# Performance work log

Hardware: AMD Instinct MI355X
Metric: run time of the kernel (lower is better)

## Reference

```python
import jax, jax.numpy as jnp
import numpy as np

B, L, F, H, HDE, E, V, MH, MW, TOUT = 64, 2, 512, 512, 512, 512, 94, 6, 40, 30
V2 = V + 2          # vocab + START/END + NULL slots
T = TOUT + 2        # decode steps
HW = MH * MW
START = V + 1
END = V + 1


def setup_inputs() -> dict:
    key = jax.random.key(0)
    ks = jax.random.split(key, 20)
    s = 0.05  # weight scale for numerical stability
    n = lambda k, shape: jax.random.normal(k, shape, jnp.float32) * s
    d = {}
    d['conv_f'] = jax.random.normal(ks[0], (B, F, MH, MW), jnp.float32)
    d['target'] = jax.random.randint(ks[1], (B, TOUT), 0, 95, dtype=jnp.int32)
    d['w_ih_en'] = n(ks[2], (L, 4 * H, F))
    d['w_hh_en'] = n(ks[3], (L, 4 * H, H))
    d['b_ih_en'] = n(ks[4], (L, 4 * H))
    d['b_hh_en'] = n(ks[5], (L, 4 * H))
    d['embed_w'] = n(ks[6], (V2, H))
    d['w_ih_de'] = n(ks[7], (L, 4 * HDE, H))
    d['w_hh_de'] = n(ks[8], (L, 4 * HDE, HDE))
    d['b_ih_de'] = n(ks[9], (L, 4 * HDE))
    d['b_hh_de'] = n(ks[10], (L, 4 * HDE))
    d['att_wh'] = n(ks[11], (E, HDE))
    d['att_bh'] = n(ks[12], (E,))
    d['att_conv_w'] = n(ks[13], (E, F, 3, 3))
    d['att_conv_b'] = n(ks[14], (E,))
    d['att_wv'] = n(ks[15], (1, E))
    d['att_bv'] = n(ks[16], (1,))
    d['out_w'] = n(ks[17], (V2, HDE + F))
    d['out_b'] = n(ks[18], (V2,))
    return d


def _lstm_cell(x, h, c, wih, whh, bih, bhh):
    # PyTorch gate order: i, f, g, o
    g = x @ wih.T + h @ whh.T + bih + bhh
    i, f, gg, o = jnp.split(g, 4, axis=-1)
    c_new = jax.nn.sigmoid(f) * c + jax.nn.sigmoid(i) * jnp.tanh(gg)
    h_new = jax.nn.sigmoid(o) * jnp.tanh(c_new)
    return h_new, c_new


def _forward(conv_f, target, w_ih_en, w_hh_en, b_ih_en, b_hh_en, embed_w,
             w_ih_de, w_hh_de, b_ih_de, b_hh_de, att_wh, att_bh,
             att_conv_w, att_conv_b, att_wv, att_bv, out_w, out_b):
    # ---- encoder: maxpool over full height, then 2-layer LSTM over width ----
    x_seq = jnp.max(conv_f, axis=2).transpose(2, 0, 1)  # [W, B, F]

    def enc_step(carry, xt):
        h, c = carry
        inp = xt
        hs, cs = [], []
        for l in range(L):
            hl, cl = _lstm_cell(inp, h[l], c[l], w_ih_en[l], w_hh_en[l],
                                b_ih_en[l], b_hh_en[l])
            inp = hl
            hs.append(hl); cs.append(cl)
        return (jnp.stack(hs), jnp.stack(cs)), inp

    z = jnp.zeros((L, B, H), conv_f.dtype)
    _, enc_out = jax.lax.scan(enc_step, (z, z), x_seq)
    holistic = enc_out[-1]  # [B, H]

    # ---- attention: conv_f embedding computed ONCE (invariant across steps) ----
    xe = jax.lax.conv_general_dilated(
        conv_f, att_conv_w, (1, 1), 'SAME',
        dimension_numbers=('NCHW', 'OIHW', 'NCHW')) + att_conv_b[None, :, None, None]
    x_em = xe.reshape(B, E, HW).transpose(0, 2, 1)       # [B, HW, E]
    cf_flat = conv_f.reshape(B, F, HW).transpose(0, 2, 1)  # [B, HW, F]

    # ---- decoder inputs: t=0 holistic, t>=1 embed(gt_with_start[:, t-1]) ----
    gt = jnp.concatenate(
        [jnp.full((B, 1), START, dtype=target.dtype), target], axis=1)  # [B, T-1]
    xs = jnp.concatenate([holistic[None], embed_w[gt.T]], axis=0)  # [T, B, H]

    def dec_step(carry, xt):
        h, c = carry
        inp = xt
        hs, cs = [], []
        for l in range(L):
            hl, cl = _lstm_cell(inp, h[l], c[l], w_ih_de[l], w_hh_de[l],
                                b_ih_de[l], b_hh_de[l])
            inp = hl
            hs.append(hl); cs.append(cl)
        hlast = inp  # [B, HDE]
        g_em = hlast @ att_wh.T + att_bh                    # [B, E]
        feat = jnp.tanh(x_em + g_em[:, None, :])            # [B, HW, E] (dropout=identity)
        e = feat @ att_wv[0] + att_bv[0]                    # [B, HW]
        alpha = jax.nn.softmax(e, axis=-1)
        att = jnp.einsum('bw,bwf->bf', alpha, cf_flat)      # [B, F]
        logits = jnp.concatenate([hlast, att], axis=-1) @ out_w.T + out_b
        scores = jax.nn.log_softmax(logits, axis=-1)        # [B, V2]
        return (jnp.stack(hs), jnp.stack(cs)), scores

    zd = jnp.zeros((B, HDE), conv_f.dtype)
    z0 = jnp.stack([zd] * L)
    _, out_tbv = jax.lax.scan(dec_step, (z0, z0), xs)  # [T, B, V2]
    out = out_tbv.transpose(1, 0, 2)                    # [B, T, V2]

    # ---- build l_target: [0, target..., 0] with first padding 0 -> END ----
    l_target = jnp.zeros((B, T), jnp.int32).at[:, 1:-1].set(target)
    j = jnp.argmax(l_target[:, 1:] == 0, axis=1) + 1  # first zero at col>=1 (always exists)
    l_target = l_target.at[jnp.arange(B), j].set(END)

    # ---- masked NLL loss ----
    lt = l_target.reshape(-1)
    nll = -out.reshape(-1, V2)[jnp.arange(B * T), lt]
    mask = (lt != 0).astype(out.dtype)
    return jnp.sum(nll * mask) / jnp.sum(mask)


def reference(conv_f, target, w_ih_en, w_hh_en, b_ih_en, b_hh_en, embed_w,
              w_ih_de, w_hh_de, b_ih_de, b_hh_de, att_wh, att_bh,
              att_conv_w, att_conv_b, att_wv, att_bv, out_w, out_b):
    return _forward(conv_f, target, w_ih_en, w_hh_en, b_ih_en, b_hh_en, embed_w,
                    w_ih_de, w_hh_de, b_ih_de, b_hh_de, att_wh, att_bh,
                    att_conv_w, att_conv_b, att_wv, att_bv, out_w, out_b)
```

## Files before the change

### kernel.cpp

```cpp
#include <hip/hip_runtime.h>

typedef __fp16 f16;
typedef __fp16 f16x4 __attribute__((ext_vector_type(4)));
typedef __fp16 f16x8 __attribute__((ext_vector_type(8)));
typedef float  f32x4 __attribute__((ext_vector_type(4)));
typedef unsigned long long ull;

#define DEV static __device__ __forceinline__

DEV f32x4 mfma16(f16x4 a, f16x4 b, f32x4 c) {
  return __builtin_amdgcn_mfma_f32_16x16x16f16(a, b, c, 0, 0, 0);
}
DEV f16x4 lo4(f16x8 v) { return __builtin_shufflevector(v, v, 0, 1, 2, 3); }
DEV f16x4 hi4(f16x8 v) { return __builtin_shufflevector(v, v, 4, 5, 6, 7); }
DEV float sigf(float x) { return 1.f / (1.f + __expf(-x)); }
DEV float tanh_(float x) { float e = __expf(2.f * x); return 1.f - 2.f / (e + 1.f); }

union U8 { float4 f4; float2 f2[2]; };
union H2 { unsigned u; f16 h[2]; };
union H4 { ull u; f16 h[4]; f16x4 v; };

#define HB 32768

DEV ull ldU(const ull* p) {
  return __hip_atomic_load(p, __ATOMIC_RELAXED, __HIP_MEMORY_SCOPE_AGENT);
}
DEV unsigned ldF(const unsigned* p) {
  return __hip_atomic_load(p, __ATOMIC_RELAXED, __HIP_MEMORY_SCOPE_AGENT);
}
DEV void stU32(unsigned* p, unsigned v) {
  __hip_atomic_store(p, v, __ATOMIC_RELAXED, __HIP_MEMORY_SCOPE_AGENT);
}
DEV void stU64(ull* p, ull v) {
  __hip_atomic_store(p, v, __ATOMIC_RELAXED, __HIP_MEMORY_SCOPE_AGENT);
}

DEV void wait8(const unsigned* line, unsigned tgt) {
  if (threadIdx.x < 8)
    while (ldF(line + threadIdx.x * 16) < tgt) {}
  __syncthreads();
}

DEV void signalDone(unsigned* line, int slot) {
  asm volatile("s_waitcnt vmcnt(0)" ::: "memory");
  __syncthreads();
  if (threadIdx.x == 0)
    __hip_atomic_fetch_add(line + slot * 16, 1u, __ATOMIC_RELAXED, __HIP_MEMORY_SCOPE_AGENT);
}

DEV void stageRow(const f16* __restrict__ s, f16* __restrict__ dstRow, int ch) {
  U8 u0, u1;
  u0.f4 = *(const float4*)s;
  u1.f4 = *(const float4*)(s + 8);
  *(float2*)(dstRow +  0 + ch * 4) = u0.f2[0];
  *(float2*)(dstRow + 16 + ch * 4) = u0.f2[1];
  *(float2*)(dstRow + 32 + ch * 4) = u1.f2[0];
  *(float2*)(dstRow + 48 + ch * 4) = u1.f2[1];
}

DEV void stageAu(const ull* __restrict__ srcU, f16 (*A)[64][72], int tid) {
  int row = tid >> 2, ch = tid & 3;
  const ull* s = srcU + row * 128 + ch * 4;
#pragma unroll
  for (int c = 0; c < 8; ++c) {
    ull d0 = ldU(s + c * 16 + 0);
    ull d1 = ldU(s + c * 16 + 1);
    ull d2 = ldU(s + c * 16 + 2);
    ull d3 = ldU(s + c * 16 + 3);
    f16* d = &A[c][row][0];
    *(ull*)(d +  0 + ch * 4) = d0;
    *(ull*)(d + 16 + ch * 4) = d1;
    *(ull*)(d + 32 + ch * 4) = d2;
    *(ull*)(d + 48 + ch * 4) = d3;
  }
}

DEV void kloop32(const f16 (*Wt)[32][72], const f16 (*A)[64][72],
                 int mh, int ns, int m16, int g4, f32x4 acc[2]) {
#pragma unroll
  for (int c = 0; c < 8; ++c) {
#pragma unroll
    for (int half = 0; half < 2; ++half) {
      f16x8 bf = *(const f16x8*)&Wt[c][ns * 16 + m16][g4 * 16 + half * 8];
      f16x4 bl = lo4(bf), bh = hi4(bf);
#pragma unroll
      for (int mt = 0; mt < 2; ++mt) {
        f16x8 af = *(const f16x8*)&A[c][mh * 32 + mt * 16 + m16][g4 * 16 + half * 8];
        acc[mt] = mfma16(lo4(af), bl, acc[mt]);
        acc[mt] = mfma16(hi4(af), bh, acc[mt]);
      }
    }
  }
}

DEV void kloop64(const f16* Wg, const f16 (*A)[64][72],
                 int nsG, int m16, int g4, f32x4 acc[4]) {
#pragma unroll
  for (int c = 0; c < 8; ++c) {
#pragma unroll
    for (int half = 0; half < 2; ++half) {
      f16x8 bf = *(const f16x8*)&Wg[((size_t)(c * 64 + nsG * 16 + m16)) * 72 + g4 * 16 + half * 8];
      f16x4 bl = lo4(bf), bh = hi4(bf);
#pragma unroll
      for (int mt = 0; mt < 4; ++mt) {
        f16x8 af = *(const f16x8*)&A[c][mt * 16 + m16][g4 * 16 + half * 8];
        acc[mt] = mfma16(lo4(af), bl, acc[mt]);
        acc[mt] = mfma16(hi4(af), bh, acc[mt]);
      }
    }
  }
}

DEV void convTile(char* smem, int tile, const f16* __restrict__ cfT,
                  const f16* __restrict__ wc9, const float* __restrict__ cb,
                  f16* __restrict__ xemH) {
  f16 (*At)[40] = (f16(*)[40])smem;
  f16 (*Bt)[40] = (f16(*)[40])(smem + 19200);
  const int t = threadIdx.x, lane = t & 63, w = t >> 6;
  const int b = tile >> 2, eb = (tile & 3) * 128;
  const int m16 = lane & 15, g4 = lane >> 4;
  f32x4 acc[15][2] = {};

  for (int kr = 0; kr < 9; ++kr) {
    int dh = kr / 3 - 1, dw = kr % 3 - 1;
    for (int f0 = 0; f0 < 512; f0 += 32) {
      __syncthreads();
      if (t < 240) {
        int hh = t / 40 + dh, ww = t % 40 + dw;
        if (hh >= 0 && hh < 6 && ww >= 0 && ww < 40) {
          const f16* s = cfT + ((size_t)(b * 240 + hh * 40 + ww) * 512 + f0);
          U8 u0, u1, u2, u3;
          u0.f4 = *(const float4*)s;        u1.f4 = *(const float4*)(s + 8);
          u2.f4 = *(const float4*)(s + 16); u3.f4 = *(const float4*)(s + 24);
          *(float2*)&At[t][ 0] = u0.f2[0];
          *(float2*)&At[t][ 8] = u0.f2[1];
          *(float2*)&At[t][16] = u1.f2[0];
          *(float2*)&At[t][24] = u1.f2[1];
          *(float2*)&At[t][ 4] = u2.f2[0];
          *(float2*)&At[t][12] = u2.f2[1];
          *(float2*)&At[t][20] = u3.f2[0];
          *(float2*)&At[t][28] = u3.f2[1];
        } else {
          float2 z = make_float2(0.f, 0.f);
          *(float2*)&At[t][ 0] = z; *(float2*)&At[t][ 8] = z;
          *(float2*)&At[t][16] = z; *(float2*)&At[t][24] = z;
          *(float2*)&At[t][ 4] = z; *(float2*)&At[t][12] = z;
          *(float2*)&At[t][20] = z; *(float2*)&At[t][28] = z;
        }
      }
      {
        int n = t >> 1, ch = t & 1;
        const f16* s = wc9 + (size_t)(eb + n) * 4608 + kr * 512 + f0 + ch * 16;
        U8 u0, u1;
        u0.f4 = *(const float4*)s; u1.f4 = *(const float4*)(s + 8);
        *(float2*)&Bt[n][ 0 + ch * 4] = u0.f2[0];
        *(float2*)&Bt[n][ 8 + ch * 4] = u0.f2[1];
        *(float2*)&Bt[n][16 + ch * 4] = u1.f2[0];
        *(float2*)&Bt[n][24 + ch * 4] = u1.f2[1];
      }
      __syncthreads();
      f16x8 b0 = *(const f16x8*)&Bt[w * 32 + m16][g4 * 8];
      f16x8 b1v = *(const f16x8*)&Bt[w * 32 + 16 + m16][g4 * 8];
      f16x4 b0l = lo4(b0), b0h = hi4(b0), b1l = lo4(b1v), b1h = hi4(b1v);
#pragma unroll
      for (int mt = 0; mt < 15; ++mt) {
        f16x8 af = *(const f16x8*)&At[mt * 16 + m16][g4 * 8];
        f16x4 al = lo4(af), ah = hi4(af);
        acc[mt][0] = mfma16(al, b0l, acc[mt][0]);
        acc[mt][1] = mfma16(al, b1l, acc[mt][1]);
        acc[mt][0] = mfma16(ah, b0h, acc[mt][0]);
        acc[mt][1] = mfma16(ah, b1h, acc[mt][1]);
      }
    }
  }
#pragma unroll
  for (int nt = 0; nt < 2; ++nt) {
    int e = eb + w * 32 + nt * 16 + m16;
    float bias = cb[e];
#pragma unroll
    for (int mt = 0; mt < 15; ++mt)
#pragma unroll
      for (int r = 0; r < 4; ++r) {
        int p = mt * 16 + g4 * 4 + r;
        xemH[((size_t)(b * 240 + p)) * 512 + e] = (f16)(acc[mt][nt][r] + bias);
      }
  }
}


__global__ void k_convert4(const float* __restrict__ src, f16* __restrict__ dst, int n4) {
  int i = blockIdx.x * 256 + threadIdx.x;
  if (i < n4) {
    float4 v = ((const float4*)src)[i];
    f16x4 o = { (f16)v.x, (f16)v.y, (f16)v.z, (f16)v.w };
    *(f16x4*)(dst + (size_t)i * 4) = o;
  }
}

__global__ void k_convW(const float* __restrict__ s0, const float* __restrict__ s1,
                        const float* __restrict__ s2, const float* __restrict__ s3,
                        f16* __restrict__ d0, f16* __restrict__ d1,
                        f16* __restrict__ d2, f16* __restrict__ d3) {
  int i = blockIdx.x * 256 + threadIdx.x;
  int sel = i >> 19, j = i & 524287;
  const float* s = sel == 0 ? s0 : sel == 1 ? s1 : sel == 2 ? s2 : s3;
  f16* d = sel == 0 ? d0 : sel == 1 ? d1 : sel == 2 ? d2 : d3;
  float4 v = ((const float4*)s)[j];
  f16x4 o = { (f16)v.x, (f16)v.y, (f16)v.z, (f16)v.w };
  *(f16x4*)(d + (size_t)j * 4) = o;
}

__global__ void k_wc9(const float* __restrict__ src, f16* __restrict__ dst) {
  int i = blockIdx.x * 256 + threadIdx.x;
  if (i < 512 * 4608) {
    int e = i / 4608, k = i % 4608;
    int rr = k / 512, f = k % 512;
    dst[i] = (f16)src[(size_t)e * 4608 + f * 9 + rr];
  }
}

__global__ __launch_bounds__(256) void k_cfmx(
    const float* __restrict__ cf, f16* __restrict__ cfT, f16* __restrict__ xseq)
{
  __shared__ float sT[64][244];
  const int tid = threadIdx.x;
  const int f0 = blockIdx.x * 64, b = blockIdx.y;
  const float* src = cf + ((size_t)b * 512 + f0) * 240;
  for (int i = tid; i < 3840; i += 256) {
    float4 v = ((const float4*)src)[i];
    int fl = i / 60, pc = (i % 60) * 4;
    sT[fl][pc] = v.x; sT[fl][pc + 1] = v.y; sT[fl][pc + 2] = v.z; sT[fl][pc + 3] = v.w;
  }
  __syncthreads();
  if (tid < 240) {
    int p = tid;
    f16* drow = cfT + ((size_t)b * 240 + p) * 512 + f0;
#pragma unroll
    for (int j = 0; j < 8; ++j) {
      f16x8 o;
#pragma unroll
      for (int k = 0; k < 8; ++k) o[k] = (f16)sT[j * 8 + k][p];
      *(f16x8*)(drow + j * 8) = o;
    }
  }
  {
    int fl = tid >> 2, wq = tid & 3;
#pragma unroll
    for (int wi = 0; wi < 10; ++wi) {
      int w = wq * 10 + wi;
      float m = sT[fl][w];
#pragma unroll
      for (int h = 1; h < 6; ++h) m = fmaxf(m, sT[fl][h * 40 + w]);
      xseq[((size_t)w * 64 + b) * 512 + f0 + fl] = (f16)m;
    }
  }
}

__global__ void k_ltarget(const int* __restrict__ target, int* __restrict__ lt) {
  int b = threadIdx.x;
  if (b >= 64) return;
  int row[32];
  row[0] = 0;
  for (int t = 1; t <= 30; ++t) row[t] = target[b * 30 + t - 1];
  row[31] = 0;
  int j = 1;
  while (row[j] != 0) ++j;
  row[j] = 95;
  for (int t = 0; t < 32; ++t) lt[b * 32 + t] = row[t];
}

__global__ void k_fill_xs(const f16* __restrict__ hol, const f16* __restrict__ emb,
                          const int* __restrict__ tgt, f16* __restrict__ xs) {
  int i = blockIdx.x * 256 + threadIdx.x;
  if (i < 32 * 64 * 512) {
    int t = i / (64 * 512), r = i % (64 * 512);
    int b = r / 512, u = r % 512;
    f16 v;
    if (t == 0) v = hol[b * 512 + u];
    else {
      int tok = (t == 1) ? 95 : tgt[b * 30 + t - 2];
      v = emb[(size_t)tok * 512 + u];
    }
    xs[i] = v;
  }
}

__global__ __launch_bounds__(256) void k_gemmX(
    const f16* __restrict__ A, const f16* __restrict__ W,
    const float* __restrict__ b1, const float* __restrict__ b2,
    f16* __restrict__ C)
{
  __shared__ f16 At[64][72];
  __shared__ f16 Bt[64][72];
  const int t = threadIdx.x, lane = t & 63, g = t >> 6;
  f32x4 acc[4] = {};
  const int m16 = lane & 15, g4 = lane >> 4;
  const size_t arow0 = (size_t)blockIdx.x * 64;

  for (int k0 = 0; k0 < 512; k0 += 64) {
    __syncthreads();
    { int row = t >> 2, ch = t & 3;
      stageRow(A + (arow0 + row) * 512 + k0 + ch * 16, &At[row][0], ch); }
    { int row = t >> 2, ch = t & 3;
      stageRow(W + ((size_t)blockIdx.y * 64 + row) * 512 + k0 + ch * 16, &Bt[row][0], ch); }
    __syncthreads();
#pragma unroll
    for (int half = 0; half < 2; ++half) {
      f16x8 bf = *(const f16x8*)&Bt[g * 16 + m16][g4 * 16 + half * 8];
      f16x4 bl = lo4(bf), bh = hi4(bf);
#pragma unroll
      for (int mt = 0; mt < 4; ++mt) {
        f16x8 af = *(const f16x8*)&At[mt * 16 + m16][g4 * 16 + half * 8];
        acc[mt] = mfma16(lo4(af), bl, acc[mt]);
        acc[mt] = mfma16(hi4(af), bh, acc[mt]);
      }
    }
  }
  int e = blockIdx.y * 64 + g * 16 + m16;
  float bias = b1[e] + b2[e];
#pragma unroll
  for (int mt = 0; mt < 4; ++mt)
#pragma unroll
    for (int r = 0; r < 4; ++r)
      C[(arow0 + mt * 16 + g4 * 4 + r) * 2048 + e] = (f16)(acc[mt][r] + bias);
}

__global__ __launch_bounds__(256) void k_gemmG(
    const f16* __restrict__ A, const f16* __restrict__ W,
    const float* __restrict__ b1, f16* __restrict__ C)
{
  __shared__ f16 At[64][72];
  __shared__ f16 Bt[64][72];
  const int t = threadIdx.x, lane = t & 63, g = t >> 6;
  f32x4 acc[4] = {};
  const int m16 = lane & 15, g4 = lane >> 4;
  const size_t arow0 = (size_t)blockIdx.x * 64;

  for (int k0 = 0; k0 < 512; k0 += 64) {
    __syncthreads();
    { int row = t >> 2, ch = t & 3;
      stageRow(A + (arow0 + row) * 512 + k0 + ch * 16, &At[row][0], ch); }
    { int row = t >> 2, ch = t & 3;
      stageRow(W + ((size_t)blockIdx.y * 64 + row) * 512 + k0 + ch * 16, &Bt[row][0], ch); }
    __syncthreads();
#pragma unroll
    for (int half = 0; half < 2; ++half) {
      f16x8 bf = *(const f16x8*)&Bt[g * 16 + m16][g4 * 16 + half * 8];
      f16x4 bl = lo4(bf), bh = hi4(bf);
#pragma unroll
      for (int mt = 0; mt < 4; ++mt) {
        f16x8 af = *(const f16x8*)&At[mt * 16 + m16][g4 * 16 + half * 8];
        acc[mt] = mfma16(lo4(af), bl, acc[mt]);
        acc[mt] = mfma16(hi4(af), bh, acc[mt]);
      }
    }
  }
  int e = blockIdx.y * 64 + g * 16 + m16;
  float bias = b1[e];
#pragma unroll
  for (int mt = 0; mt < 4; ++mt)
#pragma unroll
    for (int r = 0; r < 4; ++r)
      C[(arow0 + mt * 16 + g4 * 4 + r) * 512 + e] = (f16)(acc[mt][r] + bias);
}

__global__ __launch_bounds__(256) void k_gemmL(
    const f16* __restrict__ A, const f16* __restrict__ W,
    const float* __restrict__ bias, float* __restrict__ C)
{
  __shared__ f16 At[64][72];
  __shared__ f16 Bt[64][72];
  const int t = threadIdx.x, lane = t & 63, g = t >> 6;
  f32x4 acc[4] = {};
  const int m16 = lane & 15, g4 = lane >> 4;
  const size_t arow0 = (size_t)blockIdx.x * 64;

  for (int k0 = 0; k0 < 1024; k0 += 64) {
    __syncthreads();
    { int row = t >> 2, ch = t & 3;
      stageRow(A + (arow0 + row) * 1024 + k0 + ch * 16, &At[row][0], ch); }
    { int row = t >> 2, ch = t & 3;
      stageRow(W + ((size_t)(blockIdx.y * 64 + row)) * 1024 + k0 + ch * 16, &Bt[row][0], ch); }
    __syncthreads();
#pragma unroll
    for (int half = 0; half < 2; ++half) {
      f16x8 bf = *(const f16x8*)&Bt[g * 16 + m16][g4 * 16 + half * 8];
      f16x4 bl = lo4(bf), bh = hi4(bf);
#pragma unroll
      for (int mt = 0; mt < 4; ++mt) {
        f16x8 af = *(const f16x8*)&At[mt * 16 + m16][g4 * 16 + half * 8];
        acc[mt] = mfma16(lo4(af), bl, acc[mt]);
        acc[mt] = mfma16(hi4(af), bh, acc[mt]);
      }
    }
  }
  int e = blockIdx.y * 64 + g * 16 + m16;
  if (e < 96) {
    float be = bias[e];
#pragma unroll
    for (int mt = 0; mt < 4; ++mt)
#pragma unroll
      for (int r = 0; r < 4; ++r)
        C[(arow0 + mt * 16 + g4 * 4 + r) * 96 + e] = acc[mt][r] + be;
  }
}

__global__ __launch_bounds__(256, 1) void k_lstm(
    int T,
    const f16* __restrict__ G0, const f16* __restrict__ whh0,
    const f16* __restrict__ wih1, const f16* __restrict__ whh1,
    const float* __restrict__ bih1, const float* __restrict__ bhh1,
    f16* __restrict__ h0seq, f16* __restrict__ h1seq,
    unsigned* __restrict__ cnt,
    const f16* __restrict__ cfT, const f16* __restrict__ wc9,
    const float* __restrict__ cb, f16* __restrict__ xemH, int convBase)
{
  __shared__ __align__(16) char smem[147456];
  const int tid = threadIdx.x, lane = tid & 63, w = tid >> 6;
  const int m16 = lane & 15, g4 = lane >> 4;
  const int bid = blockIdx.x;

  if (bid >= 96) {
    convTile(smem, convBase + bid - 96, cfT, wc9, cb, xemH);
    return;
  }

  if (bid < 32) {
    f16 (*sW)[64][72] = (f16(*)[64][72])smem;
    f16 (*sA)[64][72] = (f16(*)[64][72])(smem + 73728);
    float* sG = (float*)(smem + 73728);
    const int utile = bid;
    { int r = tid >> 2, ch = tid & 3;
      int grow = (r >> 4) * 512 + utile * 16 + (r & 15);
      for (int c = 0; c < 8; ++c)
        stageRow(whh0 + (size_t)grow * 512 + c * 64 + ch * 16, &sW[c][r][0], ch);
    }
    const int pb = tid >> 2, uq = tid & 3;
    float cst[4] = {0.f, 0.f, 0.f, 0.f};
    for (int t = 0; t < T; ++t) {
      if (t > 0) wait8(cnt + (t - 1) * 128, 4);
      stageAu((const ull*)h0seq + (size_t)t * 8192, sA, tid);
      __syncthreads();
      f32x4 acc[4] = {};
      kloop64((const f16*)sW, sA, w, m16, g4, acc);
      __syncthreads();
#pragma unroll
      for (int mt = 0; mt < 4; ++mt)
#pragma unroll
        for (int r = 0; r < 4; ++r)
          sG[((size_t)w * 64 + mt * 16 + g4 * 4 + r) * 17 + m16] = acc[mt][r];
      __syncthreads();
      {
        const f16* gp = G0 + ((size_t)(t * 64 + pb)) * 2048 + utile * 16 + uq * 4;
        H4 gI, gF, gG, gO, outp;
        gI.v = *(const f16x4*)(gp);
        gF.v = *(const f16x4*)(gp + 512);
        gG.v = *(const f16x4*)(gp + 1024);
        gO.v = *(const f16x4*)(gp + 1536);
#pragma unroll
        for (int j = 0; j < 4; ++j) {
          int u = uq * 4 + j;
          float gi = sG[(0 * 64 + pb) * 17 + u] + (float)gI.h[j];
          float gf = sG[(1 * 64 + pb) * 17 + u] + (float)gF.h[j];
          float gg = sG[(2 * 64 + pb) * 17 + u] + (float)gG.h[j];
          float go = sG[(3 * 64 + pb) * 17 + u] + (float)gO.h[j];
          float cn = sigf(gf) * cst[j] + sigf(gi) * tanh_(gg);
          float hn = sigf(go) * tanh_(cn);
          cst[j] = cn;
          outp.h[j] = (f16)hn;
        }
        stU64((ull*)h0seq + (size_t)(t + 1) * 8192 + pb * 128 + utile * 4 + uq, outp.u);
      }
      signalDone(cnt + t * 128, bid & 7);
    }
  } else {
    f16 (*sW2)[8][32][72] = (f16(*)[8][32][72])smem;
    f16 (*sA)[64][72] = (f16(*)[64][72])(smem + 73728);
    float* sG = (float*)(smem + 73728);
    const int utile = bid - 32;
    const int mh = w >> 1, ns = w & 1;
    { int mat = tid >> 7;
      int r = (tid >> 2) & 31, ch = tid & 3;
      int grow = (r >> 3) * 512 + utile * 8 + (r & 7);
      const f16* Wsrc = (mat == 0) ? wih1 : whh1;
      for (int c = 0; c < 8; ++c)
        stageRow(Wsrc + (size_t)grow * 512 + c * 64 + ch * 16, &sW2[mat][c][r][0], ch);
    }
    const int pb = tid >> 2, pup = tid & 3;
    float badd[4][2];
#pragma unroll
    for (int g = 0; g < 4; ++g)
#pragma unroll
      for (int j = 0; j < 2; ++j) {
        int rr = g * 512 + utile * 8 + pup * 2 + j;
        badd[g][j] = bih1[rr] + bhh1[rr];
      }
    float cst[2] = {0.f, 0.f};
    unsigned* line1 = cnt + (size_t)T * 128;
    for (int t = 0; t < T; ++t) {
      wait8(cnt + t * 128, 4);
      stageAu((const ull*)h0seq + (size_t)(t + 1) * 8192, sA, tid);
      if (t > 0) wait8(line1 + (t - 1) * 128, 8);
      else       __syncthreads();
      ull rg[8][4];
      { const ull* s1p = (const ull*)h1seq + (size_t)t * 8192 + (tid >> 2) * 128 + (tid & 3) * 4;
#pragma unroll
        for (int c = 0; c < 8; ++c)
#pragma unroll
          for (int q = 0; q < 4; ++q) rg[c][q] = ldU(s1p + c * 16 + q);
      }
      f32x4 acc[2] = {};
      kloop32(sW2[0], sA, mh, ns, m16, g4, acc);
      __syncthreads();
      { int row = tid >> 2, ch = tid & 3;
#pragma unroll
        for (int c = 0; c < 8; ++c) {
          f16* d = &sA[c][row][0];
          *(ull*)(d +  0 + ch * 4) = rg[c][0];
          *(ull*)(d + 16 + ch * 4) = rg[c][1];
          *(ull*)(d + 32 + ch * 4) = rg[c][2];
          *(ull*)(d + 48 + ch * 4) = rg[c][3];
        }
      }
      __syncthreads();
      kloop32(sW2[1], sA, mh, ns, m16, g4, acc);
      __syncthreads();
      { int nl = ns * 16 + m16;
#pragma unroll
        for (int mt = 0; mt < 2; ++mt)
#pragma unroll
          for (int r = 0; r < 4; ++r) {
            int b = mh * 32 + mt * 16 + g4 * 4 + r;
            sG[((nl >> 3) * 64 + b) * 9 + (nl & 7)] = acc[mt][r];
          }
      }
      __syncthreads();
      {
        H2 outp;
#pragma unroll
        for (int j = 0; j < 2; ++j) {
          int u = pup * 2 + j;
          float gi = sG[(0 * 64 + pb) * 9 + u] + badd[0][j];
          float gf = sG[(1 * 64 + pb) * 9 + u] + badd[1][j];
          float gg = sG[(2 * 64 + pb) * 9 + u] + badd[2][j];
          float go = sG[(3 * 64 + pb) * 9 + u] + badd[3][j];
          float cn = sigf(gf) * cst[j] + sigf(gi) * tanh_(gg);
          float hn = sigf(go) * tanh_(cn);
          cst[j] = cn;
          outp.h[j] = (f16)hn;
        }
        stU32((unsigned*)h1seq + (size_t)(t + 1) * 16384 + pb * 256 + utile * 4 + pup, outp.u);
      }
      signalDone(line1 + t * 128, bid & 7);
    }
  }
}


__global__ __launch_bounds__(256) void k_scoreAll(
    const f16* __restrict__ xemH, const f16* __restrict__ gAll,
    const float* __restrict__ wv, float* __restrict__ esc)
{
  __shared__ f16 sX[20][512];
  const int tid = threadIdx.x, lane = tid & 63, w = tid >> 6;
  const int tile = blockIdx.x, b = blockIdx.y;
  for (int i = tid; i < 20 * 64; i += 256) {
    int row = i >> 6, seg = i & 63;
    *(f16x8*)&sX[row][seg * 8] =
        *(const f16x8*)(xemH + ((size_t)(b * 240 + tile * 20 + row)) * 512 + seg * 8);
  }
  float w8[8];
  { const float4* wp = (const float4*)(wv + lane * 8);
    float4 wa = wp[0], wb = wp[1];
    w8[0] = wa.x; w8[1] = wa.y; w8[2] = wa.z; w8[3] = wa.w;
    w8[4] = wb.x; w8[5] = wb.y; w8[6] = wb.z; w8[7] = wb.w; }
  __syncthreads();
  for (int t = 0; t < 32; ++t) {
    f16x8 gv = *(const f16x8*)(gAll + ((size_t)(t * 64 + b)) * 512 + lane * 8);
    float g8[8];
#pragma unroll
    for (int j = 0; j < 8; ++j) g8[j] = (float)gv[j];
#pragma unroll
    for (int i = 0; i < 5; ++i) {
      int rr = i * 4 + w;
      f16x8 xv = *(const f16x8*)&sX[rr][lane * 8];
      float s = 0.f;
#pragma unroll
      for (int j = 0; j < 8; ++j) s += tanh_((float)xv[j] + g8[j]) * w8[j];
#pragma unroll
      for (int m = 32; m; m >>= 1) s += __shfl_xor(s, m);
      if (lane == 0) esc[((size_t)(t * 64 + b)) * 240 + tile * 20 + rr] = s;
    }
  }
}

__global__ __launch_bounds__(256) void k_smctx(
    const float* __restrict__ esc, const f16* __restrict__ cfT,
    const f16* __restrict__ h1seq, f16* __restrict__ ctx)
{
  __shared__ float aAl[8][240];
  const int tid = threadIdx.x, lane = tid & 63, w = tid >> 6;
  const int tq = blockIdx.x, b = blockIdx.y;
  for (int half = 0; half < 2; ++half) {
    int tt = w + half * 4;
    int t = tq * 8 + tt;
    const float* er = esc + ((size_t)(t * 64 + b)) * 240;
    float v[4];
    float mx = -1e30f;
#pragma unroll
    for (int q = 0; q < 4; ++q) {
      int p = lane + q * 64;
      v[q] = (p < 240) ? er[p] : -1e30f;
      mx = fmaxf(mx, v[q]);
    }
#pragma unroll
    for (int m = 32; m; m >>= 1) mx = fmaxf(mx, __shfl_xor(mx, m));
    float sum = 0.f;
#pragma unroll
    for (int q = 0; q < 4; ++q) { v[q] = __expf(v[q] - mx); sum += v[q]; }
#pragma unroll
    for (int m = 32; m; m >>= 1) sum += __shfl_xor(sum, m);
    float inv = 1.f / sum;
#pragma unroll
    for (int q = 0; q < 4; ++q) {
      int p = lane + q * 64;
      if (p < 240) aAl[tt][p] = v[q] * inv;
    }
  }
  __syncthreads();
  float acc[8][2] = {};
  const f16* cb = cfT + (size_t)b * 240 * 512;
  for (int p = 0; p < 240; ++p) {
    H2 cw; cw.u = *(const unsigned*)(cb + (size_t)p * 512 + tid * 2);
    float c0 = (float)cw.h[0], c1 = (float)cw.h[1];
#pragma unroll
    for (int tt = 0; tt < 8; ++tt) {
      float a = aAl[tt][p];
      acc[tt][0] += a * c0;
      acc[tt][1] += a * c1;
    }
  }
#pragma unroll
  for (int tt = 0; tt < 8; ++tt) {
    int t = tq * 8 + tt;
    size_t r = (size_t)(t * 64 + b);
    H2 o; o.h[0] = (f16)acc[tt][0]; o.h[1] = (f16)acc[tt][1];
    *(unsigned*)(ctx + r * 1024 + 512 + tid * 2) = o.u;
    *(unsigned*)(ctx + r * 1024 + tid * 2) =
        *(const unsigned*)(h1seq + (size_t)(t + 1) * HB + b * 512 + tid * 2);
  }
}

__global__ void k_nllloss(const float* __restrict__ lgt, const int* __restrict__ ltg,
                          float* __restrict__ out) {
  __shared__ float sa[256], sb[256];
  int tid = threadIdx.x;
  float a = 0.f, m = 0.f;
  for (int r = tid; r < 2048; r += 256) {
    int t = r >> 6, b = r & 63;
    int tok = ltg[b * 32 + t];
    if (tok != 0) {
      const float* row = lgt + (size_t)r * 96;
      float mx = -1e30f;
      for (int j = 0; j < 96; ++j) mx = fmaxf(mx, row[j]);
      float s = 0.f;
      for (int j = 0; j < 96; ++j) s += __expf(row[j] - mx);
      a += mx + __logf(s) - row[tok];
      m += 1.f;
    }
  }
  sa[tid] = a; sb[tid] = m; __syncthreads();
  for (int s = 128; s; s >>= 1) { if (tid < s) { sa[tid] += sa[tid + s]; sb[tid] += sb[tid + s]; } __syncthreads(); }
  if (tid == 0) out[0] = sa[0] / sb[0];
}


extern "C" void kernel_launch(void* const* d_in, const int* in_sizes, int n_in,
                              void* d_out, int out_size, void* d_ws, size_t ws_size,
                              hipStream_t stream) {
  (void)in_sizes; (void)n_in; (void)out_size; (void)ws_size;
  const float* conv_f = (const float*)d_in[0];
  const int*   target = (const int*)d_in[1];
  const float* wih_en = (const float*)d_in[2];
  const float* whh_en = (const float*)d_in[3];
  const float* bih_en = (const float*)d_in[4];
  const float* bhh_en = (const float*)d_in[5];
  const float* embed  = (const float*)d_in[6];
  const float* wih_de = (const float*)d_in[7];
  const float* whh_de = (const float*)d_in[8];
  const float* bih_de = (const float*)d_in[9];
  const float* bhh_de = (const float*)d_in[10];
  const float* att_wh = (const float*)d_in[11];
  const float* att_bh = (const float*)d_in[12];
  const float* att_cw = (const float*)d_in[13];
  const float* att_cb = (const float*)d_in[14];
  const float* att_wv = (const float*)d_in[15];
  const float* out_w  = (const float*)d_in[17];
  const float* out_b  = (const float*)d_in[18];
  float* out = (float*)d_out;

  size_t o = 0;
  char* base = (char*)d_ws;
  auto take = [&](size_t bytes) -> void* {
    void* p = base + o;
    o += (bytes + 255) & ~(size_t)255;
    return p;
  };
  const size_t WSZ = (size_t)2048 * 512;
  f16* wihEn = (f16*)take(2 * WSZ * 2);
  f16* whhEn = (f16*)take(2 * WSZ * 2);
  f16* wihDe = (f16*)take(2 * WSZ * 2);
  f16* whhDe = (f16*)take(2 * WSZ * 2);
  f16* awh   = (f16*)take((size_t)512 * 512 * 2);
  f16* emb   = (f16*)take((size_t)96 * 512 * 2);
  f16* wc9   = (f16*)take((size_t)512 * 4608 * 2);
  f16* cfT   = (f16*)take((size_t)64 * 240 * 512 * 2);
  f16* xseq  = (f16*)take((size_t)40 * 64 * 512 * 2);
  f16* xs    = (f16*)take((size_t)32 * 64 * 512 * 2);
  f16* xemH  = (f16*)take((size_t)64 * 240 * 512 * 2);
  f16* outwH = (f16*)take((size_t)128 * 1024 * 2);
  f16* X0en  = (f16*)take((size_t)2560 * 2048 * 2);
  f16* X0de  = (f16*)take((size_t)2048 * 2048 * 2);
  f16* h0seqE = (f16*)take((size_t)41 * HB * 2);
  f16* h1seqE = (f16*)take((size_t)41 * HB * 2);
  f16* h0seqD = (f16*)take((size_t)33 * HB * 2);
  f16* h1seqD = (f16*)take((size_t)33 * HB * 2);
  f16* gAll   = (f16*)take((size_t)2048 * 512 * 2);
  int*   ltg   = (int*)take((size_t)2048 * 4);
  unsigned* cntE = (unsigned*)take(65536);
  unsigned* cntD = (unsigned*)take(65536);
  float* escAll = (float*)X0en;
  float* lgtAll = (float*)((char*)X0en + 4194304);
  f16*   ctxAll = X0de;

  k_convW<<<8192, 256, 0, stream>>>(wih_en, whh_en, wih_de, whh_de,
                                    wihEn, whhEn, wihDe, whhDe);
  k_convert4<<<256, 256, 0, stream>>>(att_wh, awh, 512 * 512 / 4);
  k_convert4<<<48, 256, 0, stream>>>(embed, emb, 96 * 512 / 4);
  k_convert4<<<96, 256, 0, stream>>>(out_w, outwH, 96 * 1024 / 4);
  k_wc9<<<(512 * 4608 + 255) / 256, 256, 0, stream>>>(att_cw, wc9);
  k_cfmx<<<dim3(8, 64), 256, 0, stream>>>(conv_f, cfT, xseq);
  k_ltarget<<<1, 64, 0, stream>>>(target, ltg);
  hipMemsetAsync(h0seqE, 0, (size_t)HB * 2, stream);
  hipMemsetAsync(h1seqE, 0, (size_t)HB * 2, stream);
  hipMemsetAsync(h0seqD, 0, (size_t)HB * 2, stream);
  hipMemsetAsync(h1seqD, 0, (size_t)HB * 2, stream);
  hipMemsetAsync(cntE, 0, 131072, stream);

  k_gemmX<<<dim3(40, 32), 256, 0, stream>>>(xseq, wihEn, bih_en, bhh_en, X0en);

  k_lstm<<<224, 256, 0, stream>>>(40, X0en, whhEn, wihEn + WSZ, whhEn + WSZ,
                                  bih_en + 2048, bhh_en + 2048, h0seqE, h1seqE, cntE,
                                  cfT, wc9, att_cb, xemH, 0);

  k_fill_xs<<<(32 * 64 * 512 + 255) / 256, 256, 0, stream>>>(h1seqE + (size_t)40 * HB, emb, target, xs);
  k_gemmX<<<dim3(32, 32), 256, 0, stream>>>(xs, wihDe, bih_de, bhh_de, X0de);

  k_lstm<<<224, 256, 0, stream>>>(32, X0de, whhDe, wihDe + WSZ, whhDe + WSZ,
                                  bih_de + 2048, bhh_de + 2048, h0seqD, h1seqD, cntD,
                                  cfT, wc9, att_cb, xemH, 128);

  k_gemmG<<<dim3(32, 8), 256, 0, stream>>>(h1seqD + HB, awh, att_bh, gAll);
  k_scoreAll<<<dim3(12, 64), 256, 0, stream>>>(xemH, gAll, att_wv, escAll);
  k_smctx<<<dim3(4, 64), 256, 0, stream>>>(escAll, cfT, h1seqD, ctxAll);
  k_gemmL<<<dim3(32, 2), 256, 0, stream>>>(ctxAll, outwH, out_b, lgtAll);
  k_nllloss<<<1, 256, 0, stream>>>(lgtAll, ltg, out);
}
```

Before: 906.5 us.

## Merge small prep kernels, fuse embedding gather into decoder input GEMM

```diff
diff --git a/kernel.cpp b/kernel.cpp
--- a/kernel.cpp
+++ b/kernel.cpp
@@ -188,15 +188,6 @@
 }
 
 
-__global__ void k_convert4(const float* __restrict__ src, f16* __restrict__ dst, int n4) {
-  int i = blockIdx.x * 256 + threadIdx.x;
-  if (i < n4) {
-    float4 v = ((const float4*)src)[i];
-    f16x4 o = { (f16)v.x, (f16)v.y, (f16)v.z, (f16)v.w };
-    *(f16x4*)(dst + (size_t)i * 4) = o;
-  }
-}
-
 __global__ void k_convW(const float* __restrict__ s0, const float* __restrict__ s1,
                         const float* __restrict__ s2, const float* __restrict__ s3,
                         f16* __restrict__ d0, f16* __restrict__ d1,
@@ -210,12 +201,29 @@
   *(f16x4*)(d + (size_t)j * 4) = o;
 }
 
-__global__ void k_wc9(const float* __restrict__ src, f16* __restrict__ dst) {
+__global__ void k_convS(const float* __restrict__ awhS, const float* __restrict__ embS,
+                        const float* __restrict__ outwS,
+                        f16* __restrict__ awhD, f16* __restrict__ embD,
+                        f16* __restrict__ outwD) {
   int i = blockIdx.x * 256 + threadIdx.x;
-  if (i < 512 * 4608) {
-    int e = i / 4608, k = i % 4608;
-    int rr = k / 512, f = k % 512;
-    dst[i] = (f16)src[(size_t)e * 4608 + f * 9 + rr];
+  const float* s; f16* d; int j;
+  if (i < 65536) { s = awhS; d = awhD; j = i; }
+  else if (i < 65536 + 12288) { s = embS; d = embD; j = i - 65536; }
+  else if (i < 65536 + 12288 + 24576) { s = outwS; d = outwD; j = i - 65536 - 12288; }
+  else return;
+  float4 v = ((const float4*)s)[j];
+  f16x4 o = { (f16)v.x, (f16)v.y, (f16)v.z, (f16)v.w };
+  *(f16x4*)(d + (size_t)j * 4) = o;
+}
+
+__global__ __launch_bounds__(256) void k_wc9(const float* __restrict__ src, f16* __restrict__ dst) {
+  __shared__ float s[4608];
+  const int e = blockIdx.x, tid = threadIdx.x;
+  for (int i = tid; i < 4608; i += 256) s[i] = src[(size_t)e * 4608 + i];
+  __syncthreads();
+  for (int j = tid; j < 4608; j += 256) {
+    int rr = j >> 9, f = j & 511;
+    dst[(size_t)e * 4608 + j] = (f16)s[f * 9 + rr];
   }
 }
 
@@ -256,33 +264,13 @@
   }
 }
 
-__global__ void k_ltarget(const int* __restrict__ target, int* __restrict__ lt) {
-  int b = threadIdx.x;
-  if (b >= 64) return;
-  int row[32];
-  row[0] = 0;
-  for (int t = 1; t <= 30; ++t) row[t] = target[b * 30 + t - 1];
-  row[31] = 0;
-  int j = 1;
-  while (row[j] != 0) ++j;
-  row[j] = 95;
-  for (int t = 0; t < 32; ++t) lt[b * 32 + t] = row[t];
-}
-
-__global__ void k_fill_xs(const f16* __restrict__ hol, const f16* __restrict__ emb,
-                          const int* __restrict__ tgt, f16* __restrict__ xs) {
+__global__ void k_zero(unsigned* p0, unsigned* p1, unsigned* p2,
+                       unsigned* p3, unsigned* p4, unsigned* p5) {
   int i = blockIdx.x * 256 + threadIdx.x;
-  if (i < 32 * 64 * 512) {
-    int t = i / (64 * 512), r = i % (64 * 512);
-    int b = r / 512, u = r % 512;
-    f16 v;
-    if (t == 0) v = hol[b * 512 + u];
-    else {
-      int tok = (t == 1) ? 95 : tgt[b * 30 + t - 2];
-      v = emb[(size_t)tok * 512 + u];
-    }
-    xs[i] = v;
-  }
+  int sel = i >> 14, j = i & 16383;
+  unsigned* p = sel == 0 ? p0 : sel == 1 ? p1 : sel == 2 ? p2 :
+                sel == 3 ? p3 : sel == 4 ? p4 : p5;
+  p[j] = 0;
 }
 
 __global__ __launch_bounds__(256) void k_gemmX(
@@ -325,6 +313,50 @@
       C[(arow0 + mt * 16 + g4 * 4 + r) * 2048 + e] = (f16)(acc[mt][r] + bias);
 }
 
+__global__ __launch_bounds__(256) void k_gemmXd(
+    const f16* __restrict__ x_t0, const f16* __restrict__ emb, const int* __restrict__ tgt,
+    const f16* __restrict__ W, const float* __restrict__ b1, const float* __restrict__ b2,
+    f16* __restrict__ C)
+{
+  __shared__ f16 At[64][72];
+  __shared__ f16 Bt[64][72];
+  const int t = threadIdx.x, lane = t & 63, g = t >> 6;
+  f32x4 acc[4] = {};
+  const int m16 = lane & 15, g4 = lane >> 4;
+  const int tt = blockIdx.x;
+  const size_t arow0 = (size_t)tt * 64;
+  const int row = t >> 2, ch = t & 3;
+  const f16* rowSrc;
+  if (tt == 0) rowSrc = x_t0 + (size_t)row * 512;
+  else if (tt == 1) rowSrc = emb + (size_t)95 * 512;
+  else { int tok = tgt[row * 30 + tt - 2]; rowSrc = emb + (size_t)tok * 512; }
+
+  for (int k0 = 0; k0 < 512; k0 += 64) {
+    __syncthreads();
+    stageRow(rowSrc + k0 + ch * 16, &At[row][0], ch);
+    stageRow(W + ((size_t)blockIdx.y * 64 + row) * 512 + k0 + ch * 16, &Bt[row][0], ch);
+    __syncthreads();
+#pragma unroll
+    for (int half = 0; half < 2; ++half) {
+      f16x8 bf = *(const f16x8*)&Bt[g * 16 + m16][g4 * 16 + half * 8];
+      f16x4 bl = lo4(bf), bh = hi4(bf);
+#pragma unroll
+      for (int mt = 0; mt < 4; ++mt) {
+        f16x8 af = *(const f16x8*)&At[mt * 16 + m16][g4 * 16 + half * 8];
+        acc[mt] = mfma16(lo4(af), bl, acc[mt]);
+        acc[mt] = mfma16(hi4(af), bh, acc[mt]);
+      }
+    }
+  }
+  int e = blockIdx.y * 64 + g * 16 + m16;
+  float bias = b1[e] + b2[e];
+#pragma unroll
+  for (int mt = 0; mt < 4; ++mt)
+#pragma unroll
+    for (int r = 0; r < 4; ++r)
+      C[(arow0 + mt * 16 + g4 * 4 + r) * 2048 + e] = (f16)(acc[mt][r] + bias);
+}
+
 __global__ __launch_bounds__(256) void k_gemmG(
     const f16* __restrict__ A, const f16* __restrict__ W,
     const float* __restrict__ b1, f16* __restrict__ C)
@@ -362,47 +394,6 @@
 #pragma unroll
     for (int r = 0; r < 4; ++r)
       C[(arow0 + mt * 16 + g4 * 4 + r) * 512 + e] = (f16)(acc[mt][r] + bias);
-}
-
-__global__ __launch_bounds__(256) void k_gemmL(
-    const f16* __restrict__ A, const f16* __restrict__ W,
-    const float* __restrict__ bias, float* __restrict__ C)
-{
-  __shared__ f16 At[64][72];
-  __shared__ f16 Bt[64][72];
-  const int t = threadIdx.x, lane = t & 63, g = t >> 6;
-  f32x4 acc[4] = {};
-  const int m16 = lane & 15, g4 = lane >> 4;
-  const size_t arow0 = (size_t)blockIdx.x * 64;
-
-  for (int k0 = 0; k0 < 1024; k0 += 64) {
-    __syncthreads();
-    { int row = t >> 2, ch = t & 3;
-      stageRow(A + (arow0 + row) * 1024 + k0 + ch * 16, &At[row][0], ch); }
-    { int row = t >> 2, ch = t & 3;
-      stageRow(W + ((size_t)(blockIdx.y * 64 + row)) * 1024 + k0 + ch * 16, &Bt[row][0], ch); }
-    __syncthreads();
-#pragma unroll
-    for (int half = 0; half < 2; ++half) {
-      f16x8 bf = *(const f16x8*)&Bt[g * 16 + m16][g4 * 16 + half * 8];
-      f16x4 bl = lo4(bf), bh = hi4(bf);
-#pragma unroll
-      for (int mt = 0; mt < 4; ++mt) {
-        f16x8 af = *(const f16x8*)&At[mt * 16 + m16][g4 * 16 + half * 8];
-        acc[mt] = mfma16(lo4(af), bl, acc[mt]);
-        acc[mt] = mfma16(hi4(af), bh, acc[mt]);
-      }
-    }
-  }
-  int e = blockIdx.y * 64 + g * 16 + m16;
-  if (e < 96) {
-    float be = bias[e];
-#pragma unroll
-    for (int mt = 0; mt < 4; ++mt)
-#pragma unroll
-      for (int r = 0; r < 4; ++r)
-        C[(arow0 + mt * 16 + g4 * 4 + r) * 96 + e] = acc[mt][r] + be;
-  }
 }
 
 __global__ __launch_bounds__(256, 1) void k_lstm(
@@ -438,7 +429,13 @@
     const int pb = tid >> 2, uq = tid & 3;
     float cst[4] = {0.f, 0.f, 0.f, 0.f};
     for (int t = 0; t < T; ++t) {
-      if (t > 0) wait8(cnt + (t - 1) * 128, 4);
+      if (t > 0) wait8(cnt + (size_t)(t - 1) * 128, 4);
+      const f16* gpp = G0 + (size_t)(t * 64 + pb) * 2048 + utile * 16 + uq * 4;
+      H4 gI, gF, gG, gO;
+      gI.v = *(const f16x4*)(gpp);
+      gF.v = *(const f16x4*)(gpp + 512);
+      gG.v = *(const f16x4*)(gpp + 1024);
+      gO.v = *(const f16x4*)(gpp + 1536);
       stageAu((const ull*)h0seq + (size_t)t * 8192, sA, tid);
       __syncthreads();
       f32x4 acc[4] = {};
@@ -451,12 +448,7 @@
           sG[((size_t)w * 64 + mt * 16 + g4 * 4 + r) * 17 + m16] = acc[mt][r];
       __syncthreads();
       {
-        const f16* gp = G0 + ((size_t)(t * 64 + pb)) * 2048 + utile * 16 + uq * 4;
-        H4 gI, gF, gG, gO, outp;
-        gI.v = *(const f16x4*)(gp);
-        gF.v = *(const f16x4*)(gp + 512);
-        gG.v = *(const f16x4*)(gp + 1024);
-        gO.v = *(const f16x4*)(gp + 1536);
+        H4 outp;
 #pragma unroll
         for (int j = 0; j < 4; ++j) {
           int u = uq * 4 + j;
@@ -471,7 +463,7 @@
         }
         stU64((ull*)h0seq + (size_t)(t + 1) * 8192 + pb * 128 + utile * 4 + uq, outp.u);
       }
-      signalDone(cnt + t * 128, bid & 7);
+      signalDone(cnt + (size_t)t * 128, bid & 7);
     }
   } else {
     f16 (*sW2)[8][32][72] = (f16(*)[8][32][72])smem;
@@ -498,9 +490,9 @@
     float cst[2] = {0.f, 0.f};
     unsigned* line1 = cnt + (size_t)T * 128;
     for (int t = 0; t < T; ++t) {
-      wait8(cnt + t * 128, 4);
+      wait8(cnt + (size_t)t * 128, 4);
       stageAu((const ull*)h0seq + (size_t)(t + 1) * 8192, sA, tid);
-      if (t > 0) wait8(line1 + (t - 1) * 128, 8);
+      if (t > 0) wait8(line1 + (size_t)(t - 1) * 128, 8);
       else       __syncthreads();
       ull rg[8][4];
       { const ull* s1p = (const ull*)h1seq + (size_t)t * 8192 + (tid >> 2) * 128 + (tid & 3) * 4;
@@ -551,7 +543,7 @@
         }
         stU32((unsigned*)h1seq + (size_t)(t + 1) * 16384 + pb * 256 + utile * 4 + pup, outp.u);
       }
-      signalDone(line1 + t * 128, bid & 7);
+      signalDone(line1 + (size_t)t * 128, bid & 7);
     }
   }
 }
@@ -651,10 +643,64 @@
   }
 }
 
-__global__ void k_nllloss(const float* __restrict__ lgt, const int* __restrict__ ltg,
+__global__ __launch_bounds__(256) void k_gemmL(
+    const f16* __restrict__ A, const f16* __restrict__ W,
+    const float* __restrict__ bias, float* __restrict__ C)
+{
+  __shared__ f16 At[64][72];
+  __shared__ f16 Bt[64][72];
+  const int t = threadIdx.x, lane = t & 63, g = t >> 6;
+  f32x4 acc[4] = {};
+  const int m16 = lane & 15, g4 = lane >> 4;
+  const size_t arow0 = (size_t)blockIdx.x * 64;
+
+  for (int k0 = 0; k0 < 1024; k0 += 64) {
+    __syncthreads();
+    { int row = t >> 2, ch = t & 3;
+      stageRow(A + (arow0 + row) * 1024 + k0 + ch * 16, &At[row][0], ch); }
+    { int row = t >> 2, ch = t & 3;
+      stageRow(W + ((size_t)(blockIdx.y * 64 + row)) * 1024 + k0 + ch * 16, &Bt[row][0], ch); }
+    __syncthreads();
+#pragma unroll
+    for (int half = 0; half < 2; ++half) {
+      f16x8 bf = *(const f16x8*)&Bt[g * 16 + m16][g4 * 16 + half * 8];
+      f16x4 bl = lo4(bf), bh = hi4(bf);
+#pragma unroll
+      for (int mt = 0; mt < 4; ++mt) {
+        f16x8 af = *(const f16x8*)&At[mt * 16 + m16][g4 * 16 + half * 8];
+        acc[mt] = mfma16(lo4(af), bl, acc[mt]);
+        acc[mt] = mfma16(hi4(af), bh, acc[mt]);
+      }
+    }
+  }
+  int e = blockIdx.y * 64 + g * 16 + m16;
+  if (e < 96) {
+    float be = bias[e];
+#pragma unroll
+    for (int mt = 0; mt < 4; ++mt)
+#pragma unroll
+      for (int r = 0; r < 4; ++r)
+        C[(arow0 + mt * 16 + g4 * 4 + r) * 96 + e] = acc[mt][r] + be;
+  }
+}
+
+__global__ void k_nllloss(const float* __restrict__ lgt, const int* __restrict__ target,
                           float* __restrict__ out) {
+  __shared__ int ltg[2048];
   __shared__ float sa[256], sb[256];
   int tid = threadIdx.x;
+  if (tid < 64) {
+    int b = tid;
+    int row[32];
+    row[0] = 0;
+    for (int t = 1; t <= 30; ++t) row[t] = target[b * 30 + t - 1];
+    row[31] = 0;
+    int j = 1;
+    while (row[j] != 0) ++j;
+    row[j] = 95;
+    for (int t = 0; t < 32; ++t) ltg[b * 32 + t] = row[t];
+  }
+  __syncthreads();
   float a = 0.f, m = 0.f;
   for (int r = tid; r < 2048; r += 256) {
     int t = r >> 6, b = r & 63;
@@ -716,7 +762,6 @@
   f16* wc9   = (f16*)take((size_t)512 * 4608 * 2);
   f16* cfT   = (f16*)take((size_t)64 * 240 * 512 * 2);
   f16* xseq  = (f16*)take((size_t)40 * 64 * 512 * 2);
-  f16* xs    = (f16*)take((size_t)32 * 64 * 512 * 2);
   f16* xemH  = (f16*)take((size_t)64 * 240 * 512 * 2);
   f16* outwH = (f16*)take((size_t)128 * 1024 * 2);
   f16* X0en  = (f16*)take((size_t)2560 * 2048 * 2);
@@ -726,7 +771,6 @@
   f16* h0seqD = (f16*)take((size_t)33 * HB * 2);
   f16* h1seqD = (f16*)take((size_t)33 * HB * 2);
   f16* gAll   = (f16*)take((size_t)2048 * 512 * 2);
-  int*   ltg   = (int*)take((size_t)2048 * 4);
   unsigned* cntE = (unsigned*)take(65536);
   unsigned* cntD = (unsigned*)take(65536);
   float* escAll = (float*)X0en;
@@ -735,27 +779,19 @@
 
   k_convW<<<8192, 256, 0, stream>>>(wih_en, whh_en, wih_de, whh_de,
                                     wihEn, whhEn, wihDe, whhDe);
-  k_convert4<<<256, 256, 0, stream>>>(att_wh, awh, 512 * 512 / 4);
-  k_convert4<<<48, 256, 0, stream>>>(embed, emb, 96 * 512 / 4);
-  k_convert4<<<96, 256, 0, stream>>>(out_w, outwH, 96 * 1024 / 4);
-  k_wc9<<<(512 * 4608 + 255) / 256, 256, 0, stream>>>(att_cw, wc9);
+  k_convS<<<400, 256, 0, stream>>>(att_wh, embed, out_w, awh, emb, outwH);
+  k_wc9<<<512, 256, 0, stream>>>(att_cw, wc9);
   k_cfmx<<<dim3(8, 64), 256, 0, stream>>>(conv_f, cfT, xseq);
-  k_ltarget<<<1, 64, 0, stream>>>(target, ltg);
-  hipMemsetAsync(h0seqE, 0, (size_t)HB * 2, stream);
-  hipMemsetAsync(h1seqE, 0, (size_t)HB * 2, stream);
-  hipMemsetAsync(h0seqD, 0, (size_t)HB * 2, stream);
-  hipMemsetAsync(h1seqD, 0, (size_t)HB * 2, stream);
-  hipMemsetAsync(cntE, 0, 131072, stream);
+  k_zero<<<384, 256, 0, stream>>>((unsigned*)h0seqE, (unsigned*)h1seqE,
+                                  (unsigned*)h0seqD, (unsigned*)h1seqD, cntE, cntD);
 
   k_gemmX<<<dim3(40, 32), 256, 0, stream>>>(xseq, wihEn, bih_en, bhh_en, X0en);
-
   k_lstm<<<224, 256, 0, stream>>>(40, X0en, whhEn, wihEn + WSZ, whhEn + WSZ,
                                   bih_en + 2048, bhh_en + 2048, h0seqE, h1seqE, cntE,
                                   cfT, wc9, att_cb, xemH, 0);
 
-  k_fill_xs<<<(32 * 64 * 512 + 255) / 256, 256, 0, stream>>>(h1seqE + (size_t)40 * HB, emb, target, xs);
-  k_gemmX<<<dim3(32, 32), 256, 0, stream>>>(xs, wihDe, bih_de, bhh_de, X0de);
-
+  k_gemmXd<<<dim3(32, 32), 256, 0, stream>>>(h1seqE + (size_t)40 * HB, emb, target,
+                                             wihDe, bih_de, bhh_de, X0de);
   k_lstm<<<224, 256, 0, stream>>>(32, X0de, whhDe, wihDe + WSZ, whhDe + WSZ,
                                   bih_de + 2048, bhh_de + 2048, h0seqD, h1seqD, cntD,
                                   cfT, wc9, att_cb, xemH, 128);
@@ -764,5 +800,5 @@
   k_scoreAll<<<dim3(12, 64), 256, 0, stream>>>(xemH, gAll, att_wv, escAll);
   k_smctx<<<dim3(4, 64), 256, 0, stream>>>(escAll, cfT, h1seqD, ctxAll);
   k_gemmL<<<dim3(32, 2), 256, 0, stream>>>(ctxAll, outwH, out_b, lgtAll);
-  k_nllloss<<<1, 256, 0, stream>>>(lgtAll, ltg, out);
-}
+  k_nllloss<<<1, 256, 0, stream>>>(lgtAll, target, out);
+}
```

New measurement: 856.4 us. -5.5%, faster.
